# Kernel optimization log

Measured on AMD Instinct MI355X. Metric: run time of the kernel, lower is better.

## Reference

```python
import jax, jax.numpy as jnp
import numpy as np

B, S, E, H, NF, NH, NIT = 64, 1024, 1024, 2048, 8, 4, 10
TEMP, XNOISE, LR = 1.0, 0.1, 0.1

PNAMES = ['ce_w1','ce_b1','ce_g','ce_be','ce_w2','ce_b2',
          'tp_w1','tp_b1','tp_g','tp_be','tp_w2','tp_b2',
          'en_w1','en_b1','en_g','en_be','en_w2','en_b2','en_w3','en_b3',
          'rn_w1','rn_b1','rn_g','rn_be','rn_w2','rn_b2']

def _ln(x, g, b):
    m = x.mean(-1, keepdims=True)
    v = ((x - m) ** 2).mean(-1, keepdims=True)
    return (x - m) * jax.lax.rsqrt(v + 1e-5) * g + b

def setup_inputs() -> dict:
    key = jax.random.key(0)
    ks = iter(jax.random.split(key, 40))
    w = lambda shape: jax.random.normal(next(ks), shape, jnp.float32) * 0.02
    z = lambda n: jnp.zeros((n,), jnp.float32)
    o = lambda n: jnp.ones((n,), jnp.float32)
    return {
        'current_embeddings': jax.random.normal(next(ks), (B, S, E), jnp.float32),
        'future_true': jax.random.normal(next(ks), (B, NF, E), jnp.float32),
        'ce_w1': w((E, H)), 'ce_b1': z(H), 'ce_g': o(H), 'ce_be': z(H), 'ce_w2': w((H, H)), 'ce_b2': z(H),
        'tp_w1': w((H, H)), 'tp_b1': z(H), 'tp_g': o(H), 'tp_be': z(H), 'tp_w2': w((H, E * NF)), 'tp_b2': z(E * NF),
        'en_w1': w((2 * E, H)), 'en_b1': z(H), 'en_g': o(H), 'en_be': z(H),
        'en_w2': w((H, H // 2)), 'en_b2': z(H // 2), 'en_w3': w((H // 2, 1)), 'en_b3': z(1),
        'rn_w1': w((3 * E, H)), 'rn_b1': z(H), 'rn_g': o(H), 'rn_be': z(H), 'rn_w2': w((H, E)), 'rn_b2': z(E),
    }

def _energy(emb, ce, ftrue, p):
    # emb: (..., NF, E); ce: (..., E); eval-mode (no dropout). Loop over t in
    # the original is a plain sum/NF -> vectorized over the NF axis here.
    ce_b = jnp.broadcast_to(ce[..., None, :], emb.shape)
    x = jnp.concatenate([emb, ce_b], axis=-1)            # (..., NF, 2E)
    x = jax.nn.relu(_ln(x @ p['en_w1'] + p['en_b1'], p['en_g'], p['en_be']))
    x = jax.nn.relu(x @ p['en_w2'] + p['en_b2'])
    coherence = (x @ p['en_w3'] + p['en_b3'])[..., 0].mean(-1)
    diffs = emb[..., 1:, :] - emb[..., :-1, :]
    smoothness = jnp.sqrt((diffs ** 2).sum(-1)).mean(-1)
    supervision = ((emb - ftrue) ** 2).mean((-1, -2))
    return coherence + 0.1 * smoothness + supervision

def _forward(cur, ft, p):
    ctx = cur.mean(1)                                    # (B, E)
    h = jax.nn.relu(_ln(ctx @ p['ce_w1'] + p['ce_b1'], p['ce_g'], p['ce_be']))
    ctx_h = h @ p['ce_w2'] + p['ce_b2']                  # (B, H)
    t = jax.nn.relu(_ln(ctx_h @ p['tp_w1'] + p['tp_b1'], p['tp_g'], p['tp_be']))
    traj = (t @ p['tp_w2'] + p['tp_b2']).reshape(B, 1, NF, E)
    # n_hypotheses identical deterministic trajectories + exploration noise
    noise = jax.random.normal(jax.random.key(42), (B, NH, NF, E), traj.dtype) * XNOISE
    hyp = traj + noise                                   # (B, NH, NF, E)
    ctx_e = ctx_h[:, :E]                                 # context[:, :embed_dim]

    emb = hyp.reshape(B * NH, NF, E)
    ce_flat = jnp.broadcast_to(ctx_e[:, None, :], (B, NH, E)).reshape(B * NH, E)
    ce_tiled = jnp.broadcast_to(ce_flat[:, None, :], (B * NH, NF, E))

    def refine(x, it):
        # all t-updates read the same snapshot of x -> fully vectorized over t
        prev = jnp.concatenate([x[:, :1], x[:, :-1]], axis=1)
        nxt = jnp.concatenate([x[:, 1:], x[:, -1:]], axis=1)
        neighbor = (prev + nxt) * 0.5
        inp = jnp.concatenate([x, ce_tiled, neighbor], axis=-1)   # (BH, NF, 3E)
        u = jax.nn.relu(_ln(inp @ p['rn_w1'] + p['rn_b1'], p['rn_g'], p['rn_be']))
        u = u @ p['rn_w2'] + p['rn_b2']
        x = x - LR * u
        ns = jax.random.normal(jax.random.fold_in(jax.random.key(7), it), x.shape, x.dtype) * (XNOISE * 0.1)
        x = jnp.where(it < NIT - 1, x + ns, x)  # noise on all but last iter
        return x, None

    emb, _ = jax.lax.scan(refine, emb, jnp.arange(NIT))
    refined = emb.reshape(B, NH, NF, E)

    ce_h = jnp.broadcast_to(ctx_e[:, None, :], (B, NH, E))
    ft_h = jnp.broadcast_to(ft[:, None], (B, NH, NF, E))
    energies = _energy(refined, ce_h, ft_h, p)           # (B, NH)
    probs = jax.nn.softmax(-energies / TEMP, axis=1)
    predictions = (refined * probs[..., None, None]).sum(1)  # (B, NF, E)
    return predictions

def reference(current_embeddings, future_true, ce_w1, ce_b1, ce_g, ce_be, ce_w2, ce_b2,
              tp_w1, tp_b1, tp_g, tp_be, tp_w2, tp_b2,
              en_w1, en_b1, en_g, en_be, en_w2, en_b2, en_w3, en_b3,
              rn_w1, rn_b1, rn_g, rn_be, rn_w2, rn_b2):
    p = dict(zip(PNAMES, (ce_w1, ce_b1, ce_g, ce_be, ce_w2, ce_b2,
                          tp_w1, tp_b1, tp_g, tp_be, tp_w2, tp_b2,
                          en_w1, en_b1, en_g, en_be, en_w2, en_b2, en_w3, en_b3,
                          rn_w1, rn_b1, rn_g, rn_be, rn_w2, rn_b2)))
    return _forward(current_embeddings, future_true, p)
```

## Files before the change

### kernel.cpp

```cpp
#include <hip/hip_runtime.h>
#include <hip/hip_bf16.h>
#include <stdint.h>

#define B_ 64
#define S_ 1024
#define E_ 1024
#define H_ 2048
#define NF_ 8
#define NH_ 4
#define NIT_ 10

typedef __attribute__((ext_vector_type(8))) short vshort8;
typedef __attribute__((ext_vector_type(8))) __bf16 vbf16x8;
typedef __attribute__((ext_vector_type(4))) float vfloat4;

typedef const __attribute__((address_space(1))) void* gas1_t;
typedef __attribute__((address_space(3))) void* las3_t;
__device__ __forceinline__ void gload16(const void* g, void* l) {
  __builtin_amdgcn_global_load_lds((gas1_t)g, (las3_t)l, 16, 0, 0);
}

__device__ __forceinline__ uint32_t rotl32(uint32_t v, int n) { return (v << n) | (v >> (32 - n)); }

__device__ __forceinline__ void threefry2x32(uint32_t k0, uint32_t k1, uint32_t x0, uint32_t x1,
                                             uint32_t& o0, uint32_t& o1) {
  uint32_t ks2 = k0 ^ k1 ^ 0x1BD11BDAu;
  x0 += k0; x1 += k1;
#define TF_R(r) { x0 += x1; x1 = rotl32(x1, (r)); x1 ^= x0; }
  TF_R(13) TF_R(15) TF_R(26) TF_R(6)
  x0 += k1;  x1 += ks2 + 1u;
  TF_R(17) TF_R(29) TF_R(16) TF_R(24)
  x0 += ks2; x1 += k0 + 2u;
  TF_R(13) TF_R(15) TF_R(26) TF_R(6)
  x0 += k0;  x1 += k1 + 3u;
  TF_R(17) TF_R(29) TF_R(16) TF_R(24)
  x0 += k1;  x1 += ks2 + 4u;
  TF_R(13) TF_R(15) TF_R(26) TF_R(6)
  x0 += ks2; x1 += k0 + 5u;
#undef TF_R
  o0 = x0; o1 = x1;
}

__device__ __forceinline__ uint32_t tf_bits_part(uint32_t k0, uint32_t k1, uint32_t i) {
  uint32_t o0, o1;
  threefry2x32(k0, k1, 0u, i, o0, o1);
  return o0 ^ o1;
}

__device__ __forceinline__ float erfinv_f(float x) {
  float w = -log1pf(-x * x);
  float p;
  if (w < 5.0f) {
    w -= 2.5f;
    p = 2.81022636e-08f;
    p = 3.43273939e-07f + p * w;
    p = -3.5233877e-06f + p * w;
    p = -4.39150654e-06f + p * w;
    p = 0.00021858087f + p * w;
    p = -0.00125372503f + p * w;
    p = -0.00417768164f + p * w;
    p = 0.246640727f + p * w;
    p = 1.50140941f + p * w;
  } else {
    w = sqrtf(w) - 3.0f;
    p = -0.000200214257f;
    p = 0.000100950558f + p * w;
    p = 0.00134934322f + p * w;
    p = -0.00367342844f + p * w;
    p = 0.00573950773f + p * w;
    p = -0.0076224613f + p * w;
    p = 0.00943887047f + p * w;
    p = 1.00167406f + p * w;
    p = 2.83297682f + p * w;
  }
  return p * x;
}

__device__ __forceinline__ float bits_to_normal(uint32_t bits) {
  uint32_t fb = (bits >> 9) | 0x3F800000u;
  float f = __uint_as_float(fb) - 1.0f;
  const float lo = -0.99999994f;
  float u = fmaxf(lo, f * 2.0f + lo);
  return 1.41421356f * erfinv_f(u);
}

__device__ __forceinline__ void load_bf8(const __hip_bfloat16* p, float v[8]) {
  vshort8 s = *(const vshort8*)p;
#pragma unroll
  for (int j = 0; j < 8; ++j) {
    uint32_t b = ((uint32_t)(uint16_t)s[j]) << 16;
    v[j] = __uint_as_float(b);
  }
}

__global__ __launch_bounds__(256) void colmean_partial(const float* __restrict__ cur,
                                                       float* __restrict__ part) {
  int blk = blockIdx.x;
  int b = blk >> 3, c = blk & 7;
  int t = threadIdx.x;
  const float* base = cur + ((size_t)b * S_ + (size_t)c * 128) * E_;
  float4 s = {0.f, 0.f, 0.f, 0.f};
  for (int si = 0; si < 128; ++si) {
    float4 v = *(const float4*)(base + (size_t)si * E_ + t * 4);
    s.x += v.x; s.y += v.y; s.z += v.z; s.w += v.w;
  }
  *(float4*)(part + ((size_t)c * B_ + b) * E_ + t * 4) = s;
}

__global__ __launch_bounds__(256) void colmean_final(const float* __restrict__ part,
                                                     float* __restrict__ ctx) {
  int i = blockIdx.x * 256 + threadIdx.x;
  float s = 0.f;
#pragma unroll
  for (int c = 0; c < 8; ++c) s += part[(size_t)c * (B_ * E_) + i];
  ctx[i] = s * (1.0f / S_);
}

__global__ __launch_bounds__(256) void cvt_bf16_v(const float* __restrict__ X,
                                                  __hip_bfloat16* __restrict__ Y) {
  int i = (blockIdx.x * 256 + threadIdx.x) * 8;
  float4 v0 = *(const float4*)(X + i);
  float4 v1 = *(const float4*)(X + i + 4);
  float v[8] = {v0.x, v0.y, v0.z, v0.w, v1.x, v1.y, v1.z, v1.w};
  __hip_bfloat16 o[8];
#pragma unroll
  for (int j = 0; j < 8; ++j) o[j] = __float2bfloat16(v[j]);
  *(vshort8*)&Y[i] = *(vshort8*)o;
}

struct TD {
  const float* src;
  __hip_bfloat16* dst;
  int K, N;
  float scale;
  int base;
};
struct TDArr { TD d[11]; };

__global__ __launch_bounds__(256) void transpose_batch(TDArr a) {
  __shared__ float tile[32][33];
  int b = blockIdx.x;
  int e = 0;
#pragma unroll
  for (int i = 1; i < 11; ++i)
    if (b >= a.d[i].base) e = i;
  TD t = a.d[e];
  int lt = b - t.base;
  int ntn = t.N >> 5;
  int n0 = (lt % ntn) * 32, k0 = (lt / ntn) * 32;
  int tx = threadIdx.x & 31, ty = threadIdx.x >> 5;
  for (int r = ty; r < 32; r += 8) tile[r][tx] = t.src[(size_t)(k0 + r) * t.N + n0 + tx];
  __syncthreads();
  for (int r = ty; r < 32; r += 8)
    t.dst[(size_t)(n0 + r) * t.K + k0 + tx] = __float2bfloat16(tile[tx][r] * t.scale);
}

__global__ __launch_bounds__(256) void mfma_skinny(const __hip_bfloat16* __restrict__ A,
                                                   const __hip_bfloat16* __restrict__ Bt,
                                                   float* __restrict__ part,
                                                   int N, int K, int lda, int Kc) {
  __shared__ short AS[64 * 32];
  __shared__ short BS[128 * 32];
  int t = threadIdx.x;
  int lane = t & 63, wv = t >> 6;
  int n0 = blockIdx.x * 128;
  int kbeg = blockIdx.y * Kc;
  int wn = wv * 32;
  int lrow = lane & 15, kb = (lane >> 4) * 8;
  vfloat4 acc[4][2];
#pragma unroll
  for (int i = 0; i < 4; ++i)
#pragma unroll
    for (int j = 0; j < 2; ++j) acc[i][j] = (vfloat4){0.f, 0.f, 0.f, 0.f};
  const short* Ag = (const short*)A;
  const short* Bg = (const short*)Bt;
  int arow = lane >> 2;
  int acol = (lane & 3) * 8;
  for (int k0 = kbeg; k0 < kbeg + Kc; k0 += 32) {
    gload16(Ag + (size_t)(wv * 16 + arow) * lda + k0 + acol, &AS[(wv * 16) * 32]);
#pragma unroll
    for (int c = 0; c < 2; ++c)
      gload16(Bg + (size_t)(n0 + c * 64 + wv * 16 + arow) * K + k0 + acol,
              &BS[(c * 64 + wv * 16) * 32]);
    __syncthreads();
    vbf16x8 af[4], bq[2];
#pragma unroll
    for (int i = 0; i < 4; ++i) af[i] = *(const vbf16x8*)&AS[(i * 16 + lrow) * 32 + kb];
#pragma unroll
    for (int j = 0; j < 2; ++j) bq[j] = *(const vbf16x8*)&BS[(wn + j * 16 + lrow) * 32 + kb];
#pragma unroll
    for (int i = 0; i < 4; ++i)
#pragma unroll
      for (int j = 0; j < 2; ++j)
        acc[i][j] = __builtin_amdgcn_mfma_f32_16x16x32_bf16(af[i], bq[j], acc[i][j], 0, 0, 0);
    __syncthreads();
  }
  size_t zbase = (size_t)blockIdx.y * 64;
  int crow0 = (lane >> 4) * 4;
  int ccol0 = n0 + wn + lrow;
#pragma unroll
  for (int i = 0; i < 4; ++i) {
#pragma unroll
    for (int j = 0; j < 2; ++j) {
      int col = ccol0 + j * 16;
#pragma unroll
      for (int r = 0; r < 4; ++r) {
        int rowi = i * 16 + crow0 + r;
        part[(zbase + rowi) * N + col] = acc[i][j][r];
      }
    }
  }
}

template <bool BF16OUT>
__global__ __launch_bounds__(256) void reduce_bias(const float* __restrict__ part,
                                                   const float* __restrict__ bias,
                                                   float* __restrict__ C,
                                                   __hip_bfloat16* __restrict__ Cb,
                                                   int N, int SK) {
  int i = blockIdx.x * 256 + threadIdx.x;
  int col = i & (N - 1);
  float s = bias[col];
  for (int z = 0; z < SK; ++z) s += part[(size_t)z * 64 * N + i];
  C[i] = s;
  if (BF16OUT) Cb[i] = __float2bfloat16(s);
}

__global__ __launch_bounds__(256) void reduce_cterm(const float* __restrict__ part,
                                                    const float* __restrict__ rn_b1,
                                                    const float* __restrict__ en_b1,
                                                    float* __restrict__ out, int SK) {
  int i = blockIdx.x * 256 + threadIdx.x;
  int col = i & 4095;
  float s = (col < 2048) ? rn_b1[col] : en_b1[col - 2048];
  for (int z = 0; z < SK; ++z) s += part[(size_t)z * 64 * 4096 + i];
  out[i] = s;
}

__global__ __launch_bounds__(256) void ln2048red(const float* __restrict__ part,
                                                 const float* __restrict__ bias,
                                                 const float* __restrict__ g,
                                                 const float* __restrict__ be,
                                                 __hip_bfloat16* __restrict__ out, int SK) {
  __shared__ float red[256];
  int row = blockIdx.x, t = threadIdx.x;
  int j0 = t * 8;
  float v[8];
  *(float4*)&v[0] = *(const float4*)(bias + j0);
  *(float4*)&v[4] = *(const float4*)(bias + j0 + 4);
  for (int z = 0; z < SK; ++z) {
    const float* p = part + (size_t)z * 64 * 2048 + (size_t)row * 2048 + j0;
    float4 a0 = *(const float4*)p, a1 = *(const float4*)(p + 4);
    v[0] += a0.x; v[1] += a0.y; v[2] += a0.z; v[3] += a0.w;
    v[4] += a1.x; v[5] += a1.y; v[6] += a1.z; v[7] += a1.w;
  }
  float s = 0.f;
#pragma unroll
  for (int j = 0; j < 8; ++j) s += v[j];
  red[t] = s; __syncthreads();
  for (int k = 128; k > 0; k >>= 1) { if (t < k) red[t] += red[t + k]; __syncthreads(); }
  float mean = red[0] * (1.0f / 2048.0f);
  __syncthreads();
  float s2 = 0.f;
#pragma unroll
  for (int j = 0; j < 8; ++j) { float d = v[j] - mean; s2 += d * d; }
  red[t] = s2; __syncthreads();
  for (int k = 128; k > 0; k >>= 1) { if (t < k) red[t] += red[t + k]; __syncthreads(); }
  float rstd = rsqrtf(red[0] * (1.0f / 2048.0f) + 1e-5f);
  __hip_bfloat16 o[8];
#pragma unroll
  for (int j = 0; j < 8; ++j) {
    float y = (v[j] - mean) * rstd * g[j0 + j] + be[j0 + j];
    o[j] = __float2bfloat16(fmaxf(y, 0.f));
  }
  *(vshort8*)&out[(size_t)row * 2048 + j0] = *(vshort8*)o;
}

template <int NEIGH>
__global__ __launch_bounds__(256) void ln_comb(const __hip_bfloat16* __restrict__ G,
                                               const float* __restrict__ cterm, int cstride,
                                               const float* __restrict__ g,
                                               const float* __restrict__ be,
                                               __hip_bfloat16* __restrict__ out) {
  __shared__ float red[256];
  int row = blockIdx.x, t = threadIdx.x;
  int j0 = t * 8;
  const int GS = NEIGH ? 4096 : 2048;
  float v[8];
  load_bf8(G + (size_t)row * GS + j0, v);
  {
    const float* p = cterm + (size_t)(row >> 5) * cstride + j0;
    float4 a0 = *(const float4*)p, a1 = *(const float4*)(p + 4);
    v[0] += a0.x; v[1] += a0.y; v[2] += a0.z; v[3] += a0.w;
    v[4] += a1.x; v[5] += a1.y; v[6] += a1.z; v[7] += a1.w;
  }
  if (NEIGH) {
    int f = row & 7;
    int prow = (f == 0) ? row : row - 1;
    int nrow = (f == NF_ - 1) ? row : row + 1;
    float a[8], b[8];
    load_bf8(G + (size_t)prow * 4096 + 2048 + j0, a);
    load_bf8(G + (size_t)nrow * 4096 + 2048 + j0, b);
#pragma unroll
    for (int j = 0; j < 8; ++j) v[j] += a[j] + b[j];
  }
  float s = 0.f;
#pragma unroll
  for (int j = 0; j < 8; ++j) s += v[j];
  red[t] = s; __syncthreads();
  for (int k = 128; k > 0; k >>= 1) { if (t < k) red[t] += red[t + k]; __syncthreads(); }
  float mean = red[0] * (1.0f / 2048.0f);
  __syncthreads();
  float s2 = 0.f;
#pragma unroll
  for (int j = 0; j < 8; ++j) { float d = v[j] - mean; s2 += d * d; }
  red[t] = s2; __syncthreads();
  for (int k = 128; k > 0; k >>= 1) { if (t < k) red[t] += red[t + k]; __syncthreads(); }
  float rstd = rsqrtf(red[0] * (1.0f / 2048.0f) + 1e-5f);
  __hip_bfloat16 o[8];
#pragma unroll
  for (int j = 0; j < 8; ++j) {
    float y = (v[j] - mean) * rstd * g[j0 + j] + be[j0 + j];
    o[j] = __float2bfloat16(fmaxf(y, 0.f));
  }
  *(vshort8*)&out[(size_t)row * 2048 + j0] = *(vshort8*)o;
}

template <int MODE>
__global__ __launch_bounds__(256) void gemm_gl(const __hip_bfloat16* __restrict__ A,
                                               const __hip_bfloat16* __restrict__ Bt,
                                               const float* __restrict__ bias,
                                               float* __restrict__ Cout,
                                               __hip_bfloat16* __restrict__ Cbout,
                                               int M, int N, int K, int it) {
  __shared__ short Als[128 * 64];
  __shared__ short Bls[64 * 64];
  int t = threadIdx.x;
  int lane = t & 63, wv = t >> 6;
  int n0 = blockIdx.x * 64, m0 = blockIdx.y * 128;
  int wm = (wv >> 1) * 64, wn = (wv & 1) * 32;
  int lrow = lane & 15, kb = (lane >> 4) * 8;
  vfloat4 acc[4][2];
#pragma unroll
  for (int i = 0; i < 4; ++i)
#pragma unroll
    for (int j = 0; j < 2; ++j) acc[i][j] = (vfloat4){0.f, 0.f, 0.f, 0.f};
  const short* Ag = (const short*)A;
  const short* Bg = (const short*)Bt;
  int arow = lane >> 3;
  int acol = (lane & 7) * 8;
  for (int k0 = 0; k0 < K; k0 += 64) {
#pragma unroll
    for (int c = 0; c < 4; ++c)
      gload16(Ag + (size_t)(m0 + c * 32 + wv * 8 + arow) * K + k0 + acol,
              &Als[(c * 32 + wv * 8) * 64]);
#pragma unroll
    for (int c = 0; c < 2; ++c)
      gload16(Bg + (size_t)(n0 + c * 32 + wv * 8 + arow) * K + k0 + acol,
              &Bls[(c * 32 + wv * 8) * 64]);
    __syncthreads();
    vbf16x8 af[2][4], bq[2][2];
#pragma unroll
    for (int ks = 0; ks < 2; ++ks) {
#pragma unroll
      for (int i = 0; i < 4; ++i)
        af[ks][i] = *(const vbf16x8*)&Als[(wm + i * 16 + lrow) * 64 + ks * 32 + kb];
#pragma unroll
      for (int j = 0; j < 2; ++j)
        bq[ks][j] = *(const vbf16x8*)&Bls[(wn + j * 16 + lrow) * 64 + ks * 32 + kb];
    }
#pragma unroll
    for (int ks = 0; ks < 2; ++ks)
#pragma unroll
      for (int i = 0; i < 4; ++i)
#pragma unroll
        for (int j = 0; j < 2; ++j)
          acc[i][j] = __builtin_amdgcn_mfma_f32_16x16x32_bf16(af[ks][i], bq[ks][j], acc[i][j], 0, 0, 0);
    __syncthreads();
  }
  int crow0 = m0 + wm + (lane >> 4) * 4;
  int ccol0 = n0 + wn + lrow;
  if (MODE == 2) {
    uint32_t key0 = 0, key1 = 0;
    bool addn = (it < NIT_ - 1);
    if (addn) threefry2x32(0u, 7u, 0u, (uint32_t)it, key0, key1);
#pragma unroll
    for (int i = 0; i < 4; ++i) {
#pragma unroll
      for (int j = 0; j < 2; ++j) {
        int col = ccol0 + j * 16;
        float bv = bias[col];
#pragma unroll
        for (int r = 0; r < 4; ++r) {
          uint32_t idx = (uint32_t)(crow0 + i * 16 + r) * N + col;
          float xv = Cout[idx] - 0.1f * (acc[i][j][r] + bv);
          if (addn) xv += 0.01f * bits_to_normal(tf_bits_part(key0, key1, idx));
          Cout[idx] = xv;
          Cbout[idx] = __float2bfloat16(xv);
        }
      }
    }
  } else if (MODE == 4) {
#pragma unroll
    for (int i = 0; i < 4; ++i) {
#pragma unroll
      for (int j = 0; j < 2; ++j) {
        int col = ccol0 + j * 16;
#pragma unroll
        for (int r = 0; r < 4; ++r)
          Cbout[(size_t)(crow0 + i * 16 + r) * N + col] = __float2bfloat16(acc[i][j][r]);
      }
    }
  } else {
#pragma unroll
    for (int i = 0; i < 4; ++i) {
#pragma unroll
      for (int j = 0; j < 2; ++j) {
        int col = ccol0 + j * 16;
        float bv = bias[col];
#pragma unroll
        for (int r = 0; r < 4; ++r) {
          float v = acc[i][j][r] + bv;
          if (MODE == 1) v = fmaxf(v, 0.f);
          Cout[(size_t)(crow0 + i * 16 + r) * N + col] = v;
        }
      }
    }
  }
}

__global__ __launch_bounds__(256) void reduce_traj_noise(const float* __restrict__ part,
                                                         const float* __restrict__ bias,
                                                         float* __restrict__ x,
                                                         __hip_bfloat16* __restrict__ xb,
                                                         int SK) {
  int i = blockIdx.x * 256 + threadIdx.x;
  int fe = i & 8191;
  float s = bias[fe];
  for (int z = 0; z < SK; ++z) s += part[(size_t)z * 524288 + i];
  int b = i >> 13;
#pragma unroll
  for (int h = 0; h < NH_; ++h) {
    uint32_t xi = (uint32_t)(b * 32768 + h * 8192 + fe);
    float xv = s + 0.1f * bits_to_normal(tf_bits_part(0u, 42u, xi));
    x[xi] = xv;
    xb[xi] = __float2bfloat16(xv);
  }
}

__global__ __launch_bounds__(256) void rowdot(const float* __restrict__ X2,
                                              const float* __restrict__ w3,
                                              const float* __restrict__ b3,
                                              float* __restrict__ srow) {
  __shared__ float red[256];
  int row = blockIdx.x, t = threadIdx.x;
  const float* xr = X2 + (size_t)row * E_;
  float s = 0.f;
  for (int c = t; c < E_; c += 256) s += xr[c] * w3[c];
  red[t] = s; __syncthreads();
  for (int k = 128; k > 0; k >>= 1) { if (t < k) red[t] += red[t + k]; __syncthreads(); }
  if (t == 0) srow[row] = red[0] + b3[0];
}

__global__ __launch_bounds__(256) void energy_final(const float* __restrict__ x,
                                                    const float* __restrict__ ft,
                                                    const float* __restrict__ srow,
                                                    float* __restrict__ energ) {
  __shared__ float red[256];
  int bh = blockIdx.x, t = threadIdx.x;
  int b = bh >> 2;
  const float* xb = x + (size_t)bh * (NF_ * E_);
  const float* fb = ft + (size_t)b * (NF_ * E_);
  float sup = 0.f;
  for (int i = t; i < NF_ * E_; i += 256) { float d = xb[i] - fb[i]; sup += d * d; }
  red[t] = sup; __syncthreads();
  for (int k = 128; k > 0; k >>= 1) { if (t < k) red[t] += red[t + k]; __syncthreads(); }
  float supervision = red[0] / (NF_ * E_);
  float smooth = 0.f;
  for (int d = 0; d < NF_ - 1; ++d) {
    __syncthreads();
    float sd = 0.f;
    for (int e = t; e < E_; e += 256) {
      float df = xb[(d + 1) * E_ + e] - xb[d * E_ + e];
      sd += df * df;
    }
    red[t] = sd; __syncthreads();
    for (int k = 128; k > 0; k >>= 1) { if (t < k) red[t] += red[t + k]; __syncthreads(); }
    smooth += sqrtf(red[0]);
  }
  smooth *= (1.0f / (NF_ - 1));
  if (t == 0) {
    float coh = 0.f;
    for (int f = 0; f < NF_; ++f) coh += srow[bh * NF_ + f];
    coh *= (1.0f / NF_);
    energ[bh] = coh + 0.1f * smooth + supervision;
  }
}

__global__ void softmax_probs(const float* __restrict__ energ, float* __restrict__ probs) {
  int b = threadIdx.x;
  if (b < B_) {
    float e[NH_], m = -1e30f;
#pragma unroll
    for (int h = 0; h < NH_; ++h) { e[h] = -energ[b * NH_ + h]; m = fmaxf(m, e[h]); }
    float s = 0.f, p[NH_];
#pragma unroll
    for (int h = 0; h < NH_; ++h) { p[h] = expf(e[h] - m); s += p[h]; }
#pragma unroll
    for (int h = 0; h < NH_; ++h) probs[b * NH_ + h] = p[h] / s;
  }
}

__global__ __launch_bounds__(256) void predict(const float* __restrict__ x,
                                               const float* __restrict__ probs,
                                               float* __restrict__ out) {
  int i = blockIdx.x * 256 + threadIdx.x;
  int b = i >> 13, fe = i & 8191;
  float s = 0.f;
#pragma unroll
  for (int h = 0; h < NH_; ++h) s += x[(size_t)(b * NH_ + h) * 8192 + fe] * probs[b * NH_ + h];
  out[i] = s;
}

extern "C" void kernel_launch(void* const* d_in, const int* in_sizes, int n_in,
                              void* d_out, int out_size, void* d_ws, size_t ws_size,
                              hipStream_t stream) {
  const float* cur   = (const float*)d_in[0];
  const float* ftrue = (const float*)d_in[1];
  const float* ce_w1 = (const float*)d_in[2];
  const float* ce_b1 = (const float*)d_in[3];
  const float* ce_g  = (const float*)d_in[4];
  const float* ce_be = (const float*)d_in[5];
  const float* ce_w2 = (const float*)d_in[6];
  const float* ce_b2 = (const float*)d_in[7];
  const float* tp_w1 = (const float*)d_in[8];
  const float* tp_b1 = (const float*)d_in[9];
  const float* tp_g  = (const float*)d_in[10];
  const float* tp_be = (const float*)d_in[11];
  const float* tp_w2 = (const float*)d_in[12];
  const float* tp_b2 = (const float*)d_in[13];
  const float* en_w1 = (const float*)d_in[14];
  const float* en_b1 = (const float*)d_in[15];
  const float* en_g  = (const float*)d_in[16];
  const float* en_be = (const float*)d_in[17];
  const float* en_w2 = (const float*)d_in[18];
  const float* en_b2 = (const float*)d_in[19];
  const float* en_w3 = (const float*)d_in[20];
  const float* en_b3 = (const float*)d_in[21];
  const float* rn_w1 = (const float*)d_in[22];
  const float* rn_b1 = (const float*)d_in[23];
  const float* rn_g  = (const float*)d_in[24];
  const float* rn_be = (const float*)d_in[25];
  const float* rn_w2 = (const float*)d_in[26];
  const float* rn_b2 = (const float*)d_in[27];
  (void)in_sizes; (void)n_in; (void)out_size; (void)ws_size;

  char* w = (char*)d_ws;
  size_t off = 0;
  auto alloc = [&](size_t bytes) -> void* {
    void* p = w + off;
    off += (bytes + 255) & ~(size_t)255;
    return p;
  };
  float* part   = (float*)alloc((size_t)8 * B_ * E_ * 4);
  float* ctx    = (float*)alloc((size_t)B_ * E_ * 4);
  float* g1     = (float*)alloc((size_t)B_ * H_ * 4);
  float* x      = (float*)alloc((size_t)2097152 * 4);
  float* skpart = (float*)alloc((size_t)8 * 64 * 8192 * 4);
  __hip_bfloat16* Gb = (__hip_bfloat16*)alloc((size_t)2048 * 4096 * 2);
  float* u      = (float*)alloc((size_t)2048 * 1024 * 4);
  __hip_bfloat16* ub   = (__hip_bfloat16*)alloc((size_t)2048 * 2048 * 2);
  __hip_bfloat16* x_b  = (__hip_bfloat16*)alloc((size_t)2048 * 1024 * 2);
  float* srow   = (float*)alloc((size_t)2048 * 4);
  float* energ  = (float*)alloc((size_t)256 * 4);
  float* probs  = (float*)alloc((size_t)256 * 4);
  float* ctermcat = (float*)alloc((size_t)B_ * 4096 * 4);
  __hip_bfloat16* Wcat_t  = (__hip_bfloat16*)alloc((size_t)4096 * 1024 * 2);
  __hip_bfloat16* Wbcat_t = (__hip_bfloat16*)alloc((size_t)4096 * 1024 * 2);
  __hip_bfloat16* rn_w2t = (__hip_bfloat16*)alloc((size_t)1024 * 2048 * 2);
  __hip_bfloat16* en1a_t = (__hip_bfloat16*)alloc((size_t)2048 * 1024 * 2);
  __hip_bfloat16* en_w2t = (__hip_bfloat16*)alloc((size_t)1024 * 2048 * 2);
  __hip_bfloat16* ctx_b  = (__hip_bfloat16*)alloc((size_t)B_ * E_ * 2);
  __hip_bfloat16* ctxh_b = (__hip_bfloat16*)alloc((size_t)B_ * H_ * 2);
  __hip_bfloat16* lnb    = (__hip_bfloat16*)alloc((size_t)B_ * H_ * 2);
  __hip_bfloat16* cw1t = (__hip_bfloat16*)alloc((size_t)2048 * 1024 * 2);
  __hip_bfloat16* cw2t = (__hip_bfloat16*)alloc((size_t)2048 * 2048 * 2);
  __hip_bfloat16* tw1t = (__hip_bfloat16*)alloc((size_t)2048 * 2048 * 2);
  __hip_bfloat16* tw2t = (__hip_bfloat16*)alloc((size_t)8192 * 2048 * 2);

  colmean_partial<<<512, 256, 0, stream>>>(cur, part);
  colmean_final<<<256, 256, 0, stream>>>(part, ctx);

  TDArr ta;
  int base = 0;
  auto set = [&](int idx, const float* src, __hip_bfloat16* dst, int K, int N, float sc) {
    ta.d[idx] = TD{src, dst, K, N, sc, base};
    base += (N >> 5) * (K >> 5);
  };
  set(0, rn_w1, Wcat_t, 1024, 2048, 1.0f);
  set(1, rn_w1 + (size_t)2048 * 2048, Wcat_t + (size_t)2048 * 1024, 1024, 2048, 0.5f);
  set(2, rn_w1 + (size_t)1024 * 2048, Wbcat_t, 1024, 2048, 1.0f);
  set(3, en_w1 + (size_t)1024 * 2048, Wbcat_t + (size_t)2048 * 1024, 1024, 2048, 1.0f);
  set(4, rn_w2, rn_w2t, 2048, 1024, 1.0f);
  set(5, en_w1, en1a_t, 1024, 2048, 1.0f);
  set(6, en_w2, en_w2t, 2048, 1024, 1.0f);
  set(7, ce_w1, cw1t, 1024, 2048, 1.0f);
  set(8, ce_w2, cw2t, 2048, 2048, 1.0f);
  set(9, tp_w1, tw1t, 2048, 2048, 1.0f);
  set(10, tp_w2, tw2t, 2048, 8192, 1.0f);
  transpose_batch<<<base, 256, 0, stream>>>(ta);

  cvt_bf16_v<<<32, 256, 0, stream>>>(ctx, ctx_b);
  mfma_skinny<<<dim3(16, 4), 256, 0, stream>>>(ctx_b, cw1t, skpart, 2048, 1024, 1024, 256);
  ln2048red<<<B_, 256, 0, stream>>>(skpart, ce_b1, ce_g, ce_be, lnb, 4);
  mfma_skinny<<<dim3(16, 8), 256, 0, stream>>>(lnb, cw2t, skpart, 2048, 2048, 2048, 256);
  reduce_bias<true><<<512, 256, 0, stream>>>(skpart, ce_b2, g1, ctxh_b, 2048, 8);
  mfma_skinny<<<dim3(16, 8), 256, 0, stream>>>(ctxh_b, tw1t, skpart, 2048, 2048, 2048, 256);
  ln2048red<<<B_, 256, 0, stream>>>(skpart, tp_b1, tp_g, tp_be, lnb, 8);
  mfma_skinny<<<dim3(64, 8), 256, 0, stream>>>(lnb, tw2t, skpart, 8192, 2048, 2048, 256);
  reduce_traj_noise<<<2048, 256, 0, stream>>>(skpart, tp_b2, x, x_b, 8);

  mfma_skinny<<<dim3(32, 4), 256, 0, stream>>>(ctxh_b, Wbcat_t, skpart, 4096, 1024, 2048, 256);
  reduce_cterm<<<1024, 256, 0, stream>>>(skpart, rn_b1, en_b1, ctermcat, 4);

  for (int it = 0; it < NIT_; ++it) {
    gemm_gl<4><<<dim3(64, 16), 256, 0, stream>>>(x_b, Wcat_t, nullptr, nullptr, Gb,
                                                 2048, 4096, 1024, 0);
    ln_comb<1><<<2048, 256, 0, stream>>>(Gb, ctermcat, 4096, rn_g, rn_be, ub);
    gemm_gl<2><<<dim3(16, 16), 256, 0, stream>>>(ub, rn_w2t, rn_b2, x, x_b,
                                                 2048, 1024, 2048, it);
  }

  gemm_gl<4><<<dim3(32, 16), 256, 0, stream>>>(x_b, en1a_t, nullptr, nullptr, Gb,
                                               2048, 2048, 1024, 0);
  ln_comb<0><<<2048, 256, 0, stream>>>(Gb, ctermcat + 2048, 4096, en_g, en_be, ub);
  gemm_gl<1><<<dim3(16, 16), 256, 0, stream>>>(ub, en_w2t, en_b2, u, nullptr,
                                               2048, 1024, 2048, 0);
  rowdot<<<2048, 256, 0, stream>>>(u, en_w3, en_b3, srow);
  energy_final<<<256, 256, 0, stream>>>(x, ftrue, srow, energ);
  softmax_probs<<<1, 64, 0, stream>>>(energ, probs);
  predict<<<2048, 256, 0, stream>>>(x, probs, (float*)d_out);
}
```

Before: 1.316 ms.

## Use narrower 128x32 GEMM tiles for N=1024 outputs and fuse small tail kernels

Result: faster. 1.084 ms (-17.7%).

```diff
diff --git a/kernel.cpp b/kernel.cpp
--- a/kernel.cpp
+++ b/kernel.cpp
@@ -107,25 +107,13 @@
   *(float4*)(part + ((size_t)c * B_ + b) * E_ + t * 4) = s;
 }
 
-__global__ __launch_bounds__(256) void colmean_final(const float* __restrict__ part,
-                                                     float* __restrict__ ctx) {
+__global__ __launch_bounds__(256) void colmean_final_bf(const float* __restrict__ part,
+                                                        __hip_bfloat16* __restrict__ ctxb) {
   int i = blockIdx.x * 256 + threadIdx.x;
   float s = 0.f;
 #pragma unroll
   for (int c = 0; c < 8; ++c) s += part[(size_t)c * (B_ * E_) + i];
-  ctx[i] = s * (1.0f / S_);
-}
-
-__global__ __launch_bounds__(256) void cvt_bf16_v(const float* __restrict__ X,
-                                                  __hip_bfloat16* __restrict__ Y) {
-  int i = (blockIdx.x * 256 + threadIdx.x) * 8;
-  float4 v0 = *(const float4*)(X + i);
-  float4 v1 = *(const float4*)(X + i + 4);
-  float v[8] = {v0.x, v0.y, v0.z, v0.w, v1.x, v1.y, v1.z, v1.w};
-  __hip_bfloat16 o[8];
-#pragma unroll
-  for (int j = 0; j < 8; ++j) o[j] = __float2bfloat16(v[j]);
-  *(vshort8*)&Y[i] = *(vshort8*)o;
+  ctxb[i] = __float2bfloat16(s * (1.0f / S_));
 }
 
 struct TD {
@@ -380,12 +368,92 @@
   }
   int crow0 = m0 + wm + (lane >> 4) * 4;
   int ccol0 = n0 + wn + lrow;
+  if (MODE == 4) {
+#pragma unroll
+    for (int i = 0; i < 4; ++i) {
+#pragma unroll
+      for (int j = 0; j < 2; ++j) {
+        int col = ccol0 + j * 16;
+#pragma unroll
+        for (int r = 0; r < 4; ++r)
+          Cbout[(size_t)(crow0 + i * 16 + r) * N + col] = __float2bfloat16(acc[i][j][r]);
+      }
+    }
+  } else {
+#pragma unroll
+    for (int i = 0; i < 4; ++i) {
+#pragma unroll
+      for (int j = 0; j < 2; ++j) {
+        int col = ccol0 + j * 16;
+        float bv = bias[col];
+#pragma unroll
+        for (int r = 0; r < 4; ++r) {
+          float v = acc[i][j][r] + bv;
+          if (MODE == 1) v = fmaxf(v, 0.f);
+          Cout[(size_t)(crow0 + i * 16 + r) * N + col] = v;
+        }
+      }
+    }
+  }
+}
+
+template <int MODE>
+__global__ __launch_bounds__(256) void gemm_gl32(const __hip_bfloat16* __restrict__ A,
+                                                 const __hip_bfloat16* __restrict__ Bt,
+                                                 const float* __restrict__ bias,
+                                                 float* __restrict__ Cout,
+                                                 __hip_bfloat16* __restrict__ Cbout,
+                                                 int M, int N, int K, int it) {
+  __shared__ short Als[128 * 64];
+  __shared__ short Bls[32 * 64];
+  int t = threadIdx.x;
+  int lane = t & 63, wv = t >> 6;
+  int n0 = blockIdx.x * 32, m0 = blockIdx.y * 128;
+  int wm = wv * 32;
+  int lrow = lane & 15, kb = (lane >> 4) * 8;
+  vfloat4 acc[2][2];
+#pragma unroll
+  for (int i = 0; i < 2; ++i)
+#pragma unroll
+    for (int j = 0; j < 2; ++j) acc[i][j] = (vfloat4){0.f, 0.f, 0.f, 0.f};
+  const short* Ag = (const short*)A;
+  const short* Bg = (const short*)Bt;
+  int arow = lane >> 3;
+  int acol = (lane & 7) * 8;
+  for (int k0 = 0; k0 < K; k0 += 64) {
+#pragma unroll
+    for (int c = 0; c < 4; ++c)
+      gload16(Ag + (size_t)(m0 + c * 32 + wv * 8 + arow) * K + k0 + acol,
+              &Als[(c * 32 + wv * 8) * 64]);
+    gload16(Bg + (size_t)(n0 + wv * 8 + arow) * K + k0 + acol, &Bls[(wv * 8) * 64]);
+    __syncthreads();
+    vbf16x8 af[2][2], bq[2][2];
+#pragma unroll
+    for (int ks = 0; ks < 2; ++ks) {
+#pragma unroll
+      for (int i = 0; i < 2; ++i)
+        af[ks][i] = *(const vbf16x8*)&Als[(wm + i * 16 + lrow) * 64 + ks * 32 + kb];
+#pragma unroll
+      for (int j = 0; j < 2; ++j)
+        bq[ks][j] = *(const vbf16x8*)&Bls[(j * 16 + lrow) * 64 + ks * 32 + kb];
+    }
+#pragma unroll
+    for (int ks = 0; ks < 2; ++ks)
+#pragma unroll
+      for (int i = 0; i < 2; ++i)
+#pragma unroll
+        for (int j = 0; j < 2; ++j)
+          acc[i][j] = __builtin_amdgcn_mfma_f32_16x16x32_bf16(af[ks][i], bq[ks][j], acc[i][j], 0, 0, 0);
+    __syncthreads();
+  }
+  int crow0 = m0 + wm + (lane >> 4) * 4;
+  int ccol0 = n0 + lrow;
   if (MODE == 2) {
     uint32_t key0 = 0, key1 = 0;
     bool addn = (it < NIT_ - 1);
     if (addn) threefry2x32(0u, 7u, 0u, (uint32_t)it, key0, key1);
 #pragma unroll
-    for (int i = 0; i < 4; ++i) {
+    for (int i = 0; i < 2; ++i) {
 #pragma unroll
       for (int j = 0; j < 2; ++j) {
         int col = ccol0 + j * 16;
@@ -400,20 +468,9 @@
         }
       }
     }
-  } else if (MODE == 4) {
-#pragma unroll
-    for (int i = 0; i < 4; ++i) {
-#pragma unroll
-      for (int j = 0; j < 2; ++j) {
-        int col = ccol0 + j * 16;
-#pragma unroll
-        for (int r = 0; r < 4; ++r)
-          Cbout[(size_t)(crow0 + i * 16 + r) * N + col] = __float2bfloat16(acc[i][j][r]);
-      }
-    }
   } else {
 #pragma unroll
-    for (int i = 0; i < 4; ++i) {
+    for (int i = 0; i < 2; ++i) {
 #pragma unroll
       for (int j = 0; j < 2; ++j) {
         int col = ccol0 + j * 16;
@@ -448,29 +505,24 @@
   }
 }
 
-__global__ __launch_bounds__(256) void rowdot(const float* __restrict__ X2,
-                                              const float* __restrict__ w3,
-                                              const float* __restrict__ b3,
-                                              float* __restrict__ srow) {
-  __shared__ float red[256];
-  int row = blockIdx.x, t = threadIdx.x;
-  const float* xr = X2 + (size_t)row * E_;
-  float s = 0.f;
-  for (int c = t; c < E_; c += 256) s += xr[c] * w3[c];
-  red[t] = s; __syncthreads();
-  for (int k = 128; k > 0; k >>= 1) { if (t < k) red[t] += red[t + k]; __syncthreads(); }
-  if (t == 0) srow[row] = red[0] + b3[0];
-}
-
-__global__ __launch_bounds__(256) void energy_final(const float* __restrict__ x,
-                                                    const float* __restrict__ ft,
-                                                    const float* __restrict__ srow,
-                                                    float* __restrict__ energ) {
+__global__ __launch_bounds__(256) void energy_final2(const float* __restrict__ u,
+                                                     const float* __restrict__ w3,
+                                                     const float* __restrict__ b3,
+                                                     const float* __restrict__ x,
+                                                     const float* __restrict__ ft,
+                                                     float* __restrict__ energ) {
   __shared__ float red[256];
   int bh = blockIdx.x, t = threadIdx.x;
   int b = bh >> 2;
+  const float* ur = u + (size_t)bh * (NF_ * 1024);
   const float* xb = x + (size_t)bh * (NF_ * E_);
   const float* fb = ft + (size_t)b * (NF_ * E_);
+  float c = 0.f;
+  for (int i = t; i < NF_ * 1024; i += 256) c += ur[i] * w3[i & 1023];
+  red[t] = c; __syncthreads();
+  for (int k = 128; k > 0; k >>= 1) { if (t < k) red[t] += red[t + k]; __syncthreads(); }
+  float coh = red[0] * (1.0f / NF_) + b3[0];
+  __syncthreads();
   float sup = 0.f;
   for (int i = t; i < NF_ * E_; i += 256) { float d = xb[i] - fb[i]; sup += d * d; }
   red[t] = sup; __syncthreads();
@@ -489,17 +541,16 @@
     smooth += sqrtf(red[0]);
   }
   smooth *= (1.0f / (NF_ - 1));
-  if (t == 0) {
-    float coh = 0.f;
-    for (int f = 0; f < NF_; ++f) coh += srow[bh * NF_ + f];
-    coh *= (1.0f / NF_);
-    energ[bh] = coh + 0.1f * smooth + supervision;
-  }
-}
-
-__global__ void softmax_probs(const float* __restrict__ energ, float* __restrict__ probs) {
-  int b = threadIdx.x;
-  if (b < B_) {
+  if (t == 0) energ[bh] = coh + 0.1f * smooth + supervision;
+}
+
+__global__ __launch_bounds__(256) void predict2(const float* __restrict__ x,
+                                                const float* __restrict__ energ,
+                                                float* __restrict__ out) {
+  __shared__ float pr[NH_];
+  int i = blockIdx.x * 256 + threadIdx.x;
+  int b = i >> 13, fe = i & 8191;
+  if (threadIdx.x == 0) {
     float e[NH_], m = -1e30f;
 #pragma unroll
     for (int h = 0; h < NH_; ++h) { e[h] = -energ[b * NH_ + h]; m = fmaxf(m, e[h]); }
@@ -507,18 +558,12 @@
 #pragma unroll
     for (int h = 0; h < NH_; ++h) { p[h] = expf(e[h] - m); s += p[h]; }
 #pragma unroll
-    for (int h = 0; h < NH_; ++h) probs[b * NH_ + h] = p[h] / s;
-  }
-}
-
-__global__ __launch_bounds__(256) void predict(const float* __restrict__ x,
-                                               const float* __restrict__ probs,
-                                               float* __restrict__ out) {
-  int i = blockIdx.x * 256 + threadIdx.x;
-  int b = i >> 13, fe = i & 8191;
+    for (int h = 0; h < NH_; ++h) pr[h] = p[h] / s;
+  }
+  __syncthreads();
   float s = 0.f;
 #pragma unroll
-  for (int h = 0; h < NH_; ++h) s += x[(size_t)(b * NH_ + h) * 8192 + fe] * probs[b * NH_ + h];
+  for (int h = 0; h < NH_; ++h) s += x[(size_t)(b * NH_ + h) * 8192 + fe] * pr[h];
   out[i] = s;
 }
 
@@ -563,7 +608,6 @@
     return p;
   };
   float* part   = (float*)alloc((size_t)8 * B_ * E_ * 4);
-  float* ctx    = (float*)alloc((size_t)B_ * E_ * 4);
   float* g1     = (float*)alloc((size_t)B_ * H_ * 4);
   float* x      = (float*)alloc((size_t)2097152 * 4);
   float* skpart = (float*)alloc((size_t)8 * 64 * 8192 * 4);
@@ -571,9 +615,7 @@
   float* u      = (float*)alloc((size_t)2048 * 1024 * 4);
   __hip_bfloat16* ub   = (__hip_bfloat16*)alloc((size_t)2048 * 2048 * 2);
   __hip_bfloat16* x_b  = (__hip_bfloat16*)alloc((size_t)2048 * 1024 * 2);
-  float* srow   = (float*)alloc((size_t)2048 * 4);
   float* energ  = (float*)alloc((size_t)256 * 4);
-  float* probs  = (float*)alloc((size_t)256 * 4);
   float* ctermcat = (float*)alloc((size_t)B_ * 4096 * 4);
   __hip_bfloat16* Wcat_t  = (__hip_bfloat16*)alloc((size_t)4096 * 1024 * 2);
   __hip_bfloat16* Wbcat_t = (__hip_bfloat16*)alloc((size_t)4096 * 1024 * 2);
@@ -589,7 +631,7 @@
   __hip_bfloat16* tw2t = (__hip_bfloat16*)alloc((size_t)8192 * 2048 * 2);
 
   colmean_partial<<<512, 256, 0, stream>>>(cur, part);
-  colmean_final<<<256, 256, 0, stream>>>(part, ctx);
+  colmean_final_bf<<<256, 256, 0, stream>>>(part, ctx_b);
 
   TDArr ta;
   int base = 0;
@@ -610,7 +652,6 @@
   set(10, tp_w2, tw2t, 2048, 8192, 1.0f);
   transpose_batch<<<base, 256, 0, stream>>>(ta);
 
-  cvt_bf16_v<<<32, 256, 0, stream>>>(ctx, ctx_b);
   mfma_skinny<<<dim3(16, 4), 256, 0, stream>>>(ctx_b, cw1t, skpart, 2048, 1024, 1024, 256);
   ln2048red<<<B_, 256, 0, stream>>>(skpart, ce_b1, ce_g, ce_be, lnb, 4);
   mfma_skinny<<<dim3(16, 8), 256, 0, stream>>>(lnb, cw2t, skpart, 2048, 2048, 2048, 256);
@@ -627,17 +668,15 @@
     gemm_gl<4><<<dim3(64, 16), 256, 0, stream>>>(x_b, Wcat_t, nullptr, nullptr, Gb,
                                                  2048, 4096, 1024, 0);
     ln_comb<1><<<2048, 256, 0, stream>>>(Gb, ctermcat, 4096, rn_g, rn_be, ub);
-    gemm_gl<2><<<dim3(16, 16), 256, 0, stream>>>(ub, rn_w2t, rn_b2, x, x_b,
-                                                 2048, 1024, 2048, it);
+    gemm_gl32<2><<<dim3(32, 16), 256, 0, stream>>>(ub, rn_w2t, rn_b2, x, x_b,
+                                                   2048, 1024, 2048, it);
   }
 
   gemm_gl<4><<<dim3(32, 16), 256, 0, stream>>>(x_b, en1a_t, nullptr, nullptr, Gb,
                                                2048, 2048, 1024, 0);
   ln_comb<0><<<2048, 256, 0, stream>>>(Gb, ctermcat + 2048, 4096, en_g, en_be, ub);
-  gemm_gl<1><<<dim3(16, 16), 256, 0, stream>>>(ub, en_w2t, en_b2, u, nullptr,
-                                               2048, 1024, 2048, 0);
-  rowdot<<<2048, 256, 0, stream>>>(u, en_w3, en_b3, srow);
-  energy_final<<<256, 256, 0, stream>>>(x, ftrue, srow, energ);
-  softmax_probs<<<1, 64, 0, stream>>>(energ, probs);
-  predict<<<2048, 256, 0, stream>>>(x, probs, (float*)d_out);
-}
+  gemm_gl32<1><<<dim3(32, 16), 256, 0, stream>>>(ub, en_w2t, en_b2, u, nullptr,
+                                                 2048, 1024, 2048, 0);
+  energy_final2<<<256, 256, 0, stream>>>(u, en_w3, en_b3, x, ftrue, energ);
+  predict2<<<2048, 256, 0, stream>>>(x, energ, (float*)d_out);
+}
```
